# Kernel optimization log

Hardware: AMD Instinct MI355X
Metric: run time of the kernel (lower is better)

## Reference

```python
import jax, jax.numpy as jnp
import numpy as np

T, B, A, N = 64, 32, 8, 16
E, H = 64, 4
LSTM_I, LSTM_H = 128, 128
D_SELF = 16 + 9 * (32 - 2) + 4  # 290


def setup_inputs() -> dict:
    key = jax.random.key(0)
    ks = jax.random.split(key, 24)
    f32 = jnp.float32
    d = {}
    d["x_agent"] = jax.random.normal(ks[0], (T, B, A, 16), f32)
    d["x_lidar"] = jax.random.normal(ks[1], (T, B, A, 32), f32)
    d["x_safe_zone"] = jax.random.normal(ks[2], (T, B, A, 4), f32)
    d["x_ent0"] = jax.random.normal(ks[3], (T, B, A, N, 12), f32)
    d["x_ent1"] = jax.random.normal(ks[4], (T, B, A, N, 8), f32)
    d["mask0"] = jax.random.randint(ks[5], (T, B, A, N), 0, 2).astype(jnp.int32)
    d["mask1"] = jax.random.randint(ks[6], (T, B, A, N), 0, 2).astype(jnp.int32)
    d["done"] = jax.random.randint(ks[7], (T, B), 0, 2).astype(jnp.int32)
    d["actions"] = jax.random.randint(ks[8], (T, B, A, 2), 0, 5).astype(jnp.int32)
    w = lambda k, s: jax.random.normal(k, s, f32) * 0.05
    z = lambda s: jnp.zeros(s, f32)
    d["conv_w"] = w(ks[9], (9, 1, 3)); d["conv_b"] = z((9,))
    d["self_w"] = w(ks[10], (E, 2 * D_SELF)); d["self_b"] = z((E,))
    d["ent0_w"] = w(ks[11], (E, 12 + D_SELF)); d["ent0_b"] = z((E,))
    d["ent1_w"] = w(ks[12], (E, 8 + D_SELF)); d["ent1_b"] = z((E,))
    d["in_proj_w"] = w(ks[13], (3 * E, E)); d["in_proj_b"] = z((3 * E,))
    d["out_proj_w"] = w(ks[14], (E, E)); d["out_proj_b"] = z((E,))
    d["sa_w"] = w(ks[15], (E, E)); d["sa_b"] = z((E,))
    d["pool_w"] = w(ks[16], (LSTM_I, D_SELF + E)); d["pool_b"] = z((LSTM_I,))
    d["w_ih"] = w(ks[17], (4 * LSTM_H, LSTM_I)); d["w_hh"] = w(ks[18], (4 * LSTM_H, LSTM_H))
    d["b_ih"] = z((4 * LSTM_H,)); d["b_hh"] = z((4 * LSTM_H,))
    d["head0_w"] = w(ks[19], (5, LSTM_H)); d["head0_b"] = z((5,))
    d["head1_w"] = w(ks[20], (5, LSTM_H)); d["head1_b"] = z((5,))
    return d


def _forward(x_agent, x_lidar, x_safe_zone, x_ent0, x_ent1,
             conv_w, conv_b, self_w, self_b, ent0_w, ent0_b, ent1_w, ent1_b,
             in_proj_w, in_proj_b, out_proj_w, out_proj_b, sa_w, sa_b,
             pool_w, pool_b, w_ih, w_hh, b_ih, b_hh,
             head0_w, head0_b, head1_w, head1_b,
             mask0, mask1, done, actions):
    f32 = jnp.float32
    lin = lambda x, w, b: x @ w.T + b
    # lidar conv: Conv1d(1,9,k=3), padding=0 (padding_mode='circular' is inert with padding=0)
    xl = x_lidar.reshape(T * B * A, 1, 32)
    zl = jax.lax.conv_general_dilated(xl, conv_w, (1,), 'VALID',
                                      dimension_numbers=('NCH', 'OIH', 'NCH'))
    zl = jax.nn.relu(zl + conv_b[None, :, None]).reshape(T, B, A, -1)  # (T,B,A,270)
    x_self = jnp.concatenate([x_agent, zl, x_safe_zone], axis=-1)  # (T,B,A,290)
    z_self = jax.nn.relu(lin(jnp.concatenate([x_self, x_self], -1), self_w, self_b))[..., None, :]
    xs = jnp.broadcast_to(x_self[..., None, :], (T, B, A, N, D_SELF))
    z0 = jax.nn.relu(lin(jnp.concatenate([x_ent0, xs], -1), ent0_w, ent0_b))
    z1 = jax.nn.relu(lin(jnp.concatenate([x_ent1, xs], -1), ent1_w, ent1_b))
    z_ent = jnp.concatenate([z_self, z0, z1], axis=-2)  # (T,B,A,M,E), M = 1+2N = 33
    M = z_ent.shape[-2]
    mask = jnp.concatenate([jnp.ones((T, B, A, 1), f32),
                            mask0.astype(f32), mask1.astype(f32)], axis=-1)  # (T,B,A,M)
    # self-attention over entities, flattened over (T,B,A)
    S = T * B * A
    zf = z_ent.reshape(S, M, E)
    q, k, v = jnp.split(zf @ in_proj_w.T + in_proj_b, 3, axis=-1)
    Dh = E // H
    q = q.reshape(S, M, H, Dh); k = k.reshape(S, M, H, Dh); v = v.reshape(S, M, H, Dh)
    sc = jnp.einsum('sqhd,skhd->shqk', q, k) / np.float32(np.sqrt(Dh))
    valid = mask.reshape(S, M) > 0
    sc = jnp.where(valid[:, None, None, :], sc, jnp.float32(-1e9))
    attn = jax.nn.softmax(sc, axis=-1)
    o = jnp.einsum('shqk,skhd->sqhd', attn, v).reshape(S, M, E)
    o = (o @ out_proj_w.T + out_proj_b).reshape(T, B, A, M, E)
    res = z_ent + jax.nn.relu(lin(o, sa_w, sa_b))
    z_pool = jnp.mean(res * mask[..., None], axis=-2)  # torch.mean over entity dim (divide by M)
    zin = jax.nn.relu(lin(jnp.concatenate([x_self, z_pool], -1), pool_w, pool_b))  # (T,B,A,128)
    # LSTM scan with done-based state resets (PyTorch gate order i,f,g,o)
    zin_f = zin.reshape(T, B * A, LSTM_I)
    done_f = jnp.repeat(done.astype(f32), A, axis=-1)  # (T, B*A)
    def step(carry, inp):
        h, c = carry
        x_t, d_t = inp
        keep = (1.0 - d_t)[:, None]
        h = h * keep
        c = c * keep
        g = x_t @ w_ih.T + b_ih + h @ w_hh.T + b_hh
        i, f, gg, og = jnp.split(g, 4, axis=-1)
        c = jax.nn.sigmoid(f) * c + jax.nn.sigmoid(i) * jnp.tanh(gg)
        h = jax.nn.sigmoid(og) * jnp.tanh(c)
        return (h, c), h
    h0 = jnp.zeros((B * A, LSTM_H), f32)
    c0 = jnp.zeros((B * A, LSTM_H), f32)
    _, hs = jax.lax.scan(step, (h0, c0), (zin_f, done_f))
    z_lstm = hs.reshape(T, B, A, LSTM_H)
    # categorical heads: per-head logprob of given action and entropy
    lps, ents = [], []
    for i, (hw, hb) in enumerate(((head0_w, head0_b), (head1_w, head1_b))):
        logp = jax.nn.log_softmax(lin(z_lstm, hw, hb), axis=-1)
        p = jnp.exp(logp)
        ents.append(-(p * logp).sum(-1))
        lps.append(jnp.take_along_axis(logp, actions[..., i:i + 1], axis=-1)[..., 0])
    logprobs = lps[0] * lps[1]  # .prod(dim=-1) over heads as in source
    entropies = jnp.stack(ents, axis=-1)
    return logprobs, entropies


def reference(x_agent, x_lidar, x_safe_zone, x_ent0, x_ent1, mask0, mask1, done, actions,
              conv_w, conv_b, self_w, self_b, ent0_w, ent0_b, ent1_w, ent1_b,
              in_proj_w, in_proj_b, out_proj_w, out_proj_b, sa_w, sa_b,
              pool_w, pool_b, w_ih, w_hh, b_ih, b_hh,
              head0_w, head0_b, head1_w, head1_b):
    logprobs, entropies = _forward(x_agent, x_lidar, x_safe_zone, x_ent0, x_ent1,
                                   conv_w, conv_b, self_w, self_b, ent0_w, ent0_b,
                                   ent1_w, ent1_b, in_proj_w, in_proj_b, out_proj_w,
                                   out_proj_b, sa_w, sa_b, pool_w, pool_b,
                                   w_ih, w_hh, b_ih, b_hh,
                                   head0_w, head0_b, head1_w, head1_b,
                                   mask0, mask1, done, actions)
    return (actions, logprobs, entropies)
```

## Files before the change

kernel.cpp:

```cpp
#include <hip/hip_runtime.h>
#include <hip/hip_bf16.h>
#include <math.h>

#define T_DIM 64
#define B_DIM 32
#define S_TOT 16384
#define BA 256
#define FN_SB 16

#define ACT_OFF 0
#define LP_OFF 32768
#define ENT_OFF 49152

typedef __attribute__((ext_vector_type(8))) short short8;
typedef __attribute__((ext_vector_type(4))) float f32x4;
typedef unsigned int uint32;

__device__ __forceinline__ float sigf(float x) { return 1.0f / (1.0f + expf(-x)); }
__device__ __forceinline__ float bf2f(unsigned short u) {
    union { unsigned int i; float f; } a; a.i = ((unsigned int)u) << 16; return a.f;
}
__device__ __forceinline__ uint32 pkbf(float a, float b) {
    __hip_bfloat16 ha = __float2bfloat16(a), hb = __float2bfloat16(b);
    return (uint32)(*(unsigned short*)&ha) | ((uint32)(*(unsigned short*)&hb) << 16);
}
__device__ __forceinline__ short f2bs(float v) {
    __hip_bfloat16 h = __float2bfloat16(v); return *(short*)&h;
}
__device__ __forceinline__ int pswz(int row) { return (((row & 3) ^ ((row >> 2) & 3)) << 4); }

__global__ __launch_bounds__(256) void k_cvt2(
    const float* __restrict__ inp_w, const float* __restrict__ outp_w,
    const float* __restrict__ outp_b, const float* __restrict__ sa_w,
    const float* __restrict__ sa_b, const float* __restrict__ self_w,
    const float* __restrict__ pool_w, const float* __restrict__ ent0_w,
    const float* __restrict__ ent1_w, const float* __restrict__ w_ih,
    const float* __restrict__ w_hh,
    short* __restrict__ wq, short* __restrict__ Wf,
    short* __restrict__ We0, short* __restrict__ We1,
    short* __restrict__ wos, float* __restrict__ bos,
    short* __restrict__ wihb, short* __restrict__ whhb,
    short* __restrict__ wp2)
{
    int i = blockIdx.x * 256 + threadIdx.x;
    if (i < 12288) wq[i] = f2bs(inp_w[i]);
    if (i < 65536) { wihb[i] = f2bs(w_ih[i]); whhb[i] = f2bs(w_hh[i]); }
    if (i < 8192) { int c = i >> 6, k = i & 63; wp2[i] = f2bs(pool_w[(size_t)c * 354 + 290 + k]); }
    if (i < 4096) {
        int c = i >> 6, k = i & 63;
        float s = 0.f;
        for (int j = 0; j < 64; ++j) s = fmaf(sa_w[c * 64 + j], outp_w[j * 64 + k], s);
        wos[i] = f2bs(s);
    }
    if (i < 64) {
        float s = sa_b[i];
        for (int j = 0; j < 64; ++j) s = fmaf(sa_w[i * 64 + j], outp_b[j], s);
        bos[i] = s;
    }
    if (i < 1024) {
        int cp = i >> 4, k = i & 15;
        int ct = cp >> 4, lr2 = cp & 15;
        int e = 32 * (ct >> 1) + 2 * lr2 + (ct & 1);
        We0[i] = f2bs(k < 12 ? ent0_w[e * 302 + k] : 0.f);
        We1[i] = f2bs(k < 8 ? ent1_w[e * 298 + k] : 0.f);
    }
    if (i < 102400) {
        int c = i / 320, k = i - c * 320;
        float v = 0.f;
        if (k < 290) {
            if (c < 64) v = self_w[c * 580 + k] + self_w[c * 580 + 290 + k];
            else if (c < 192) v = pool_w[(size_t)(c - 64) * 354 + k];
            else if (c < 256) v = ent0_w[(c - 192) * 302 + 12 + k];
            else v = ent1_w[(c - 256) * 298 + 8 + k];
        }
        Wf[i] = f2bs(v);
    }
}

#define FN_XSB 0
#define FN_XP0 16384
#define FN_XP1 20736
#define FN_TOTAL 25088

__global__ __launch_bounds__(256, 4) void k_frontN(
    const float* __restrict__ xag, const float* __restrict__ xlid,
    const float* __restrict__ xsz, const float* __restrict__ xe0,
    const float* __restrict__ xe1,
    const float* __restrict__ conv_w, const float* __restrict__ conv_b,
    const float* __restrict__ self_b, const float* __restrict__ ent0_b,
    const float* __restrict__ ent1_b,
    const short* __restrict__ Wf, const short* __restrict__ We0,
    const short* __restrict__ We1,
    __hip_bfloat16* __restrict__ z_ent, float* __restrict__ zin_x)
{
    extern __shared__ char smem[];
    char* xsb = smem + FN_XSB;
    float* xp0f = (float*)(smem + FN_XP0);
    float* xp1f = (float*)(smem + FN_XP1);
    char* ae = smem + FN_XSB;
    float* lidf = (float*)(smem + FN_XP0);

    const int tid = threadIdx.x;
    const int s0 = blockIdx.x * FN_SB;
    const int wv = __builtin_amdgcn_readfirstlane(tid >> 6);
    const int l = tid & 63;
    const int lr = l & 15;
    const int lg = l >> 4;

    for (int i = tid; i < FN_SB * 32; i += 256) {
        int d = i & 31, sl = i >> 5;
        lidf[d * 18 + sl] = xlid[(size_t)s0 * 32 + i];
    }
    for (int i = tid; i < FN_SB * 16; i += 256) {
        int sl = i >> 4, d = i & 15;
        *(short*)(xsb + ((sl * 640 + d * 2) ^ ((sl & 7) << 4))) = f2bs(xag[(size_t)s0 * 16 + i]);
    }
    for (int i = tid; i < FN_SB * 4; i += 256) {
        int sl = i >> 2, d = i & 3;
        *(short*)(xsb + ((sl * 640 + (286 + d) * 2) ^ ((sl & 7) << 4))) = f2bs(xsz[(size_t)s0 * 4 + i]);
    }
    for (int i = tid; i < FN_SB * 30; i += 256) {
        int sl = i / 30, d = 290 + (i - (i / 30) * 30);
        *(short*)(xsb + ((sl * 640 + d * 2) ^ ((sl & 7) << 4))) = 0;
    }
    __syncthreads();
    #pragma unroll
    for (int c = 0; c < 9; ++c) {
        float w0 = conv_w[c * 3], w1 = conv_w[c * 3 + 1], w2 = conv_w[c * 3 + 2];
        float bb = conv_b[c];
        for (int i = tid; i < 30 * FN_SB; i += 256) {
            int p = i >> 4, sl = i & 15;
            float v = bb + w0 * lidf[p * 18 + sl] + w1 * lidf[(p + 1) * 18 + sl]
                    + w2 * lidf[(p + 2) * 18 + sl];
            *(short*)(xsb + ((sl * 640 + (16 + c * 30 + p) * 2) ^ ((sl & 7) << 4))) = f2bs(fmaxf(v, 0.f));
        }
    }
    __syncthreads();

    f32x4 acc[5];
    #pragma unroll
    for (int c = 0; c < 5; ++c) acc[c] = (f32x4){0.f, 0.f, 0.f, 0.f};

    for (int kk = 0; kk < 10; ++kk) {
        short8 af = *(const short8*)(xsb + ((lr * 640 + kk * 64 + lg * 16) ^ ((lr & 7) << 4)));
        short8 bf[5];
        #pragma unroll
        for (int c = 0; c < 5; ++c) {
            int col = (wv * 5 + c) * 16 + lr;
            bf[c] = *(const short8*)(Wf + (size_t)col * 320 + kk * 32 + lg * 8);
        }
        #pragma unroll
        for (int c = 0; c < 5; ++c)
            acc[c] = __builtin_amdgcn_mfma_f32_16x16x32_bf16(af, bf[c], acc[c], 0, 0, 0);
    }

    #pragma unroll
    for (int c = 0; c < 5; ++c) {
        int ct = wv * 5 + c;
        int gc = ct * 16 + lr;
        int rowb = lg * 4;
        f32x4 a = acc[c];
        if (ct * 16 < 64) {
            float bias = self_b[gc];
            #pragma unroll
            for (int r = 0; r < 4; ++r)
                z_ent[(size_t)(s0 + rowb + r) * 2112 + gc] = __float2bfloat16(fmaxf(a[r] + bias, 0.f));
        } else if (ct * 16 < 192) {
            int r2 = gc - 64;
            #pragma unroll
            for (int r = 0; r < 4; ++r)
                zin_x[(size_t)(s0 + rowb + r) * 128 + r2] = a[r];
        } else if (ct * 16 < 256) {
            float bias = ent0_b[gc - 192];
            #pragma unroll
            for (int r = 0; r < 4; ++r)
                xp0f[(rowb + r) * 68 + (gc - 192)] = a[r] + bias;
        } else {
            float bias = ent1_b[gc - 256];
            #pragma unroll
            for (int r = 0; r < 4; ++r)
                xp1f[(rowb + r) * 68 + (gc - 256)] = a[r] + bias;
        }
    }
    __syncthreads();

    {
        short8 bz = {0, 0, 0, 0, 0, 0, 0, 0};
        short8 be[4];
        #pragma unroll
        for (int ct = 0; ct < 4; ++ct) {
            int col = ct * 16 + lr;
            short8 bv = *(const short8*)(We0 + col * 16 + (lg & 1) * 8);
            be[ct] = (lg < 2) ? bv : bz;
        }
        for (int i = tid; i < 4096; i += 256) ((uint32*)ae)[i] = 0;
        __syncthreads();
        {
            int sl = tid >> 4, n = tid & 15;
            int row = sl * 16 + n;
            int sw = (row & 3) << 4;
            const float4* src = (const float4*)(xe0 + (size_t)(s0 + sl) * 192 + n * 12);
            float4 v0 = src[0], v1 = src[1], v2 = src[2];
            *(uint32*)(ae + ((row * 64 + 0) ^ sw))  = pkbf(v0.x, v0.y);
            *(uint32*)(ae + ((row * 64 + 4) ^ sw))  = pkbf(v0.z, v0.w);
            *(uint32*)(ae + ((row * 64 + 8) ^ sw))  = pkbf(v1.x, v1.y);
            *(uint32*)(ae + ((row * 64 + 12) ^ sw)) = pkbf(v1.z, v1.w);
            *(uint32*)(ae + ((row * 64 + 16) ^ sw)) = pkbf(v2.x, v2.y);
            *(uint32*)(ae + ((row * 64 + 20) ^ sw)) = pkbf(v2.z, v2.w);
        }
        __syncthreads();
        #pragma unroll
        for (int j = 0; j < 4; ++j) {
            int gs = wv * 4 + j;
            int row = gs * 16 + lr;
            short8 af = *(const short8*)(ae + ((row * 64 + lg * 16) ^ ((row & 3) << 4)));
            f32x4 a2[4];
            #pragma unroll
            for (int ct = 0; ct < 4; ++ct) {
                f32x4 z = {0.f, 0.f, 0.f, 0.f};
                a2[ct] = __builtin_amdgcn_mfma_f32_16x16x32_bf16(af, be[ct], z, 0, 0, 0);
            }
            #pragma unroll
            for (int t = 0; t < 2; ++t) {
                int e0 = 32 * t + 2 * lr;
                float xv0 = xp0f[gs * 68 + e0];
                float xv1 = xp0f[gs * 68 + e0 + 1];
                #pragma unroll
                for (int r = 0; r < 4; ++r) {
                    int n = lg * 4 + r;
                    float v0 = fmaxf(a2[2 * t][r] + xv0, 0.f);
                    float v1 = fmaxf(a2[2 * t + 1][r] + xv1, 0.f);
                    *(uint32*)((char*)z_ent + ((size_t)(s0 + gs) * 2112 + (1 + n) * 64 + e0) * 2) = pkbf(v0, v1);
                }
            }
        }
        __syncthreads();
    }

    {
        short8 bz = {0, 0, 0, 0, 0, 0, 0, 0};
        short8 be[4];
        #pragma unroll
        for (int ct = 0; ct < 4; ++ct) {
            int col = ct * 16 + lr;
            short8 bv = *(const short8*)(We1 + col * 16 + (lg & 1) * 8);
            be[ct] = (lg < 2) ? bv : bz;
        }
        for (int i = tid; i < 4096; i += 256) ((uint32*)ae)[i] = 0;
        __syncthreads();
        {
            int sl = tid >> 4, n = tid & 15;
            int row = sl * 16 + n;
            int sw = (row & 3) << 4;
            const float4* src = (const float4*)(xe1 + (size_t)(s0 + sl) * 128 + n * 8);
            float4 v0 = src[0], v1 = src[1];
            *(uint32*)(ae + ((row * 64 + 0) ^ sw))  = pkbf(v0.x, v0.y);
            *(uint32*)(ae + ((row * 64 + 4) ^ sw))  = pkbf(v0.z, v0.w);
            *(uint32*)(ae + ((row * 64 + 8) ^ sw))  = pkbf(v1.x, v1.y);
            *(uint32*)(ae + ((row * 64 + 12) ^ sw)) = pkbf(v1.z, v1.w);
        }
        __syncthreads();
        #pragma unroll
        for (int j = 0; j < 4; ++j) {
            int gs = wv * 4 + j;
            int row = gs * 16 + lr;
            short8 af = *(const short8*)(ae + ((row * 64 + lg * 16) ^ ((row & 3) << 4)));
            f32x4 a2[4];
            #pragma unroll
            for (int ct = 0; ct < 4; ++ct) {
                f32x4 z = {0.f, 0.f, 0.f, 0.f};
                a2[ct] = __builtin_amdgcn_mfma_f32_16x16x32_bf16(af, be[ct], z, 0, 0, 0);
            }
            #pragma unroll
            for (int t = 0; t < 2; ++t) {
                int e0 = 32 * t + 2 * lr;
                float xv0 = xp1f[gs * 68 + e0];
                float xv1 = xp1f[gs * 68 + e0 + 1];
                #pragma unroll
                for (int r = 0; r < 4; ++r) {
                    int n = lg * 4 + r;
                    float v0 = fmaxf(a2[2 * t][r] + xv0, 0.f);
                    float v1 = fmaxf(a2[2 * t + 1][r] + xv1, 0.f);
                    *(uint32*)((char*)z_ent + ((size_t)(s0 + gs) * 2112 + (17 + n) * 64 + e0) * 2) = pkbf(v0, v1);
                }
            }
        }
    }
}

#define AG_QB   0
#define AG_KB   4224
#define AG_VT   8448
#define AG_PW   12544
#define AG_P32  16640
#define AG_V32  17408
#define AG_MSK  17664
#define AG_TOTAL 17824

__global__ __launch_bounds__(256, 8) void k_attnG(
    const __hip_bfloat16* __restrict__ z_ent,
    const int* __restrict__ mask0, const int* __restrict__ mask1,
    const short* __restrict__ wqkvb, const float* __restrict__ inp_b,
    const short* __restrict__ wos_g, const float* __restrict__ bos_g,
    float* __restrict__ pooled_ws)
{
    extern __shared__ char smem[];
    char*  Qb  = smem + AG_QB;
    char*  Kb  = smem + AG_KB;
    char*  Vt  = smem + AG_VT;
    char*  Pw  = smem + AG_PW;
    float* P32 = (float*)(smem + AG_P32);
    float* V32 = (float*)(smem + AG_V32);
    float* msk = (float*)(smem + AG_MSK);
    char*  ob  = Qb;

    const int tid = threadIdx.x;
    const int s = blockIdx.x;
    const short* zg = (const short*)(z_ent + (size_t)s * 2112);

    if (tid < 16) msk[1 + tid] = (float)mask0[(size_t)s * 16 + tid];
    else if (tid < 32) msk[17 + (tid - 16)] = (float)mask1[(size_t)s * 16 + (tid - 16)];
    else if (tid == 32) msk[0] = 1.0f;

    const int wv = __builtin_amdgcn_readfirstlane(tid >> 6);
    const int l  = tid & 63;
    const int lr = l & 15;
    const int lg = l >> 4;

    {
        short8 bw[3][2]; float bias[3];
        #pragma unroll
        for (int c = 0; c < 3; ++c) {
            int col = (wv * 3 + c) * 16 + lr;
            bw[c][0] = *(const short8*)(wqkvb + col * 64 + lg * 8);
            bw[c][1] = *(const short8*)(wqkvb + col * 64 + 32 + lg * 8);
            bias[c] = inp_b[col];
        }
        for (int rt = 0; rt < 3; ++rt) {
            int arow = rt * 16 + lr;
            if (arow > 32) arow = 32;
            short8 a0 = *(const short8*)(zg + arow * 64 + lg * 8);
            short8 a1 = *(const short8*)(zg + arow * 64 + 32 + lg * 8);
            #pragma unroll
            for (int c = 0; c < 3; ++c) {
                f32x4 acc = {0.f, 0.f, 0.f, 0.f};
                acc = __builtin_amdgcn_mfma_f32_16x16x32_bf16(a0, bw[c][0], acc, 0, 0, 0);
                acc = __builtin_amdgcn_mfma_f32_16x16x32_bf16(a1, bw[c][1], acc, 0, 0, 0);
                int col = (wv * 3 + c) * 16 + lr;
                int rb = rt * 16 + lg * 4;
                #pragma unroll
                for (int r = 0; r < 4; ++r) {
                    int q = rb + r;
                    if (q < 33) {
                        float val = acc[r] + bias[c];
                        if (col < 64) {
                            int h = col >> 4, d = col & 15;
                            *(short*)(Qb + ((h * 33 + q) * 32) + d * 2) = f2bs(val);
                        } else if (col < 128) {
                            int kc = col - 64; int h = kc >> 4, d = kc & 15;
                            *(short*)(Kb + ((h * 33 + q) * 32) + d * 2) = f2bs(val);
                        } else {
                            int vc = col - 128; int h = vc >> 4, d = vc & 15;
                            if (q < 32)
                                *(short*)(Vt + (h * 16 + d) * 64 + ((q * 2) ^ pswz(d))) = f2bs(val);
                            else
                                V32[h * 16 + d] = val;
                        }
                    }
                }
            }
        }
    }
    __syncthreads();

    uint32 pk[3][4];
    {
        const short8 zero8 = {0, 0, 0, 0, 0, 0, 0, 0};
        short8 kf[3];
        #pragma unroll
        for (int t = 0; t < 3; ++t)
            kf[t] = (lg < 2) ? *(const short8*)(Kb + ((wv * 33 + t * 16 + lr) * 32) + lg * 16) : zero8;
        float mk0 = msk[lr];
        float mk1 = msk[16 + lr];
        float mk2 = (lr == 0) ? msk[32] : 0.f;
        float sc0 = mk0 * 0.25f, bo0 = (mk0 - 1.f) * 40.f;
        float sc1 = mk1 * 0.25f, bo1 = (mk1 - 1.f) * 40.f;
        float sc2 = mk2 * 0.25f, bo2 = (mk2 - 1.f) * 40.f;
        #pragma unroll
        for (int qt = 0; qt < 3; ++qt) {
            short8 qf = (lg < 2) ? *(const short8*)(Qb + ((wv * 33 + qt * 16 + lr) * 32) + lg * 16) : zero8;
            f32x4 z = {0.f, 0.f, 0.f, 0.f};
            f32x4 S0 = __builtin_amdgcn_mfma_f32_16x16x32_bf16(qf, kf[0], z, 0, 0, 0);
            f32x4 S1 = __builtin_amdgcn_mfma_f32_16x16x32_bf16(qf, kf[1], z, 0, 0, 0);
            f32x4 S2 = __builtin_amdgcn_mfma_f32_16x16x32_bf16(qf, kf[2], z, 0, 0, 0);
            #pragma unroll
            for (int r = 0; r < 4; ++r) {
                float e0 = __expf(fmaf(S0[r], sc0, bo0));
                float e1 = __expf(fmaf(S1[r], sc1, bo1));
                float e2 = __expf(fmaf(S2[r], sc2, bo2));
                float sm = e0 + e1 + e2;
                sm += __shfl_xor(sm, 1);
                sm += __shfl_xor(sm, 2);
                sm += __shfl_xor(sm, 4);
                sm += __shfl_xor(sm, 8);
                float inv = 1.0f / sm;
                pk[qt][r] = pkbf(e0 * inv, e1 * inv);
                if (lr == 0) P32[wv * 48 + qt * 16 + lg * 4 + r] = e2 * inv;
            }
        }
    }
    __syncthreads();

    {
        short8 vf = *(const short8*)(Vt + (wv * 16 + lr) * 64 + ((lg * 16) ^ pswz(lr)));
        float v32reg = V32[wv * 16 + lr];
        f32x4 C[3];
        #pragma unroll
        for (int qt = 0; qt < 3; ++qt) {
            #pragma unroll
            for (int r = 0; r < 4; ++r) {
                int ql = lg * 4 + r;
                uint32 p = pk[qt][r];
                char* prow = Pw + wv * 1024 + ql * 64;
                int sz = pswz(ql);
                *(short*)(prow + ((lr * 2) ^ sz)) = (short)(p & 0xffffu);
                *(short*)(prow + (((16 + lr) * 2) ^ sz)) = (short)(p >> 16);
            }
            short8 pf = *(const short8*)(Pw + wv * 1024 + lr * 64 + ((lg * 16) ^ pswz(lr)));
            f32x4 z = {0.f, 0.f, 0.f, 0.f};
            C[qt] = __builtin_amdgcn_mfma_f32_16x16x32_bf16(pf, vf, z, 0, 0, 0);
        }
        #pragma unroll
        for (int qt = 0; qt < 3; ++qt) {
            #pragma unroll
            for (int r = 0; r < 4; ++r) {
                int q = qt * 16 + lg * 4 + r;
                if (q <= 32) {
                    float cv = C[qt][r] + P32[wv * 48 + q] * v32reg;
                    *(short*)(ob + ((q * 128 + (wv * 16 + lr) * 2) ^ ((q & 7) << 4))) = f2bs(cv);
                }
            }
        }
    }
    __syncthreads();

    {
        int col = wv * 16 + lr;
        short8 b0 = *(const short8*)(wos_g + col * 64 + lg * 8);
        short8 b1 = *(const short8*)(wos_g + col * 64 + 32 + lg * 8);
        float bias = bos_g[col];
        float ps = 0.f;
        for (int rt = 0; rt < 3; ++rt) {
            int arow = rt * 16 + lr;
            int sw = (arow & 7) << 4;
            short8 a0 = *(const short8*)(ob + ((arow * 128 + lg * 16) ^ sw));
            short8 a1 = *(const short8*)(ob + ((arow * 128 + 64 + lg * 16) ^ sw));
            f32x4 acc = {0.f, 0.f, 0.f, 0.f};
            acc = __builtin_amdgcn_mfma_f32_16x16x32_bf16(a0, b0, acc, 0, 0, 0);
            acc = __builtin_amdgcn_mfma_f32_16x16x32_bf16(a1, b1, acc, 0, 0, 0);
            int rb = rt * 16 + lg * 4;
            #pragma unroll
            for (int r = 0; r < 4; ++r) {
                int row = rb + r;
                if (row < 33) {
                    float zev = bf2f(*(const unsigned short*)(zg + row * 64 + col));
                    ps += msk[row] * (zev + fmaxf(acc[r] + bias, 0.f));
                }
            }
        }
        ps += __shfl_xor(ps, 16); ps += __shfl_xor(ps, 32);
        if (lg == 0) pooled_ws[(size_t)s * 64 + col] = ps * (1.0f / 33.0f);
    }
}

__global__ __launch_bounds__(256, 2) void k_zinx(
    const float* __restrict__ pooled_ws, const float* __restrict__ zin_x,
    const short* __restrict__ wp2, const float* __restrict__ pool_b,
    const short* __restrict__ wihb, const float* __restrict__ b_ih,
    const float* __restrict__ b_hh, short* __restrict__ xp)
{
    extern __shared__ char smem[];
    char* A1 = smem;
    char* zt = smem + 8192;
    const int tid = threadIdx.x;
    const size_t r0 = (size_t)blockIdx.x * 64;

    for (int i = tid; i < 2048; i += 256) {
        int sl = i >> 5, dp = i & 31;
        float2 v = ((const float2*)(pooled_ws + (r0 + sl) * 64))[dp];
        *(uint32*)(A1 + ((sl * 128 + dp * 4) ^ ((sl & 7) << 4))) = pkbf(v.x, v.y);
    }
    __syncthreads();

    const int wv = __builtin_amdgcn_readfirstlane(tid >> 6);
    const int l = tid & 63;
    const int lr = l & 15;
    const int lg = l >> 4;

    #pragma unroll
    for (int c = 0; c < 2; ++c) {
        int col = (wv * 2 + c) * 16 + lr;
        short8 bf0 = *(const short8*)(wp2 + col * 64 + lg * 8);
        short8 bf1 = *(const short8*)(wp2 + col * 64 + 32 + lg * 8);
        float bias = pool_b[col];
        #pragma unroll
        for (int rt = 0; rt < 4; ++rt) {
            int row16 = rt * 16 + lr;
            short8 a0 = *(const short8*)(A1 + ((row16 * 128 + lg * 16) ^ ((row16 & 7) << 4)));
            short8 a1 = *(const short8*)(A1 + ((row16 * 128 + 64 + lg * 16) ^ ((row16 & 7) << 4)));
            f32x4 acc = {0.f, 0.f, 0.f, 0.f};
            acc = __builtin_amdgcn_mfma_f32_16x16x32_bf16(a0, bf0, acc, 0, 0, 0);
            acc = __builtin_amdgcn_mfma_f32_16x16x32_bf16(a1, bf1, acc, 0, 0, 0);
            #pragma unroll
            for (int r = 0; r < 4; ++r) {
                int row = rt * 16 + lg * 4 + r;
                float v = fmaxf(acc[r] + bias + zin_x[(r0 + row) * 128 + col], 0.f);
                *(short*)(zt + ((row * 256 + col * 2) ^ ((row & 7) << 4))) = f2bs(v);
            }
        }
    }
    __syncthreads();

    short8 af[4][4];
    #pragma unroll
    for (int rt = 0; rt < 4; ++rt)
        #pragma unroll
        for (int kc = 0; kc < 4; ++kc) {
            int row = rt * 16 + lr;
            af[rt][kc] = *(const short8*)(zt + ((row * 256 + kc * 64 + lg * 16) ^ ((row & 7) << 4)));
        }

    for (int ct8 = 0; ct8 < 8; ++ct8) {
        int ct = wv * 8 + ct8;
        int col = ct * 16 + lr;
        short8 bf[4];
        #pragma unroll
        for (int kc = 0; kc < 4; ++kc)
            bf[kc] = *(const short8*)(wihb + (size_t)col * 128 + kc * 32 + lg * 8);
        float bias = b_ih[col] + b_hh[col];
        int g = col >> 7, j = col & 127;
        #pragma unroll
        for (int rt = 0; rt < 4; ++rt) {
            f32x4 acc = {0.f, 0.f, 0.f, 0.f};
            #pragma unroll
            for (int kc = 0; kc < 4; ++kc)
                acc = __builtin_amdgcn_mfma_f32_16x16x32_bf16(af[rt][kc], bf[kc], acc, 0, 0, 0);
            #pragma unroll
            for (int r = 0; r < 4; ++r)
                xp[(r0 + rt * 16 + lg * 4 + r) * 512 + j * 4 + g] = f2bs(acc[r] + bias);
        }
    }
}

__global__ __launch_bounds__(512, 1) void k_lstm2(
    const short* __restrict__ xp, const short* __restrict__ whhb,
    const int* __restrict__ done, float* __restrict__ h_all)
{
    __shared__ short hl[16 * 128];
    __shared__ float keepl[64 * 16];
    const int tid = threadIdx.x;
    const int s0 = blockIdx.x * 16;
    const int wv = __builtin_amdgcn_readfirstlane(tid >> 6);
    const int l = tid & 63;
    const int lr = l & 15;
    const int lg = l >> 4;

    for (int i = tid; i < 1024; i += 512) {
        int t = i >> 4, ls = i & 15;
        keepl[i] = done[t * 32 + ((s0 + ls) >> 3)] ? 0.f : 1.f;
    }
    for (int i = tid; i < 1024; i += 512) ((uint32*)hl)[i] = 0;

    short8 bf[4][4];
    #pragma unroll
    for (int gi = 0; gi < 4; ++gi) {
        int col = (gi * 8 + wv) * 16 + lr;
        #pragma unroll
        for (int kc = 0; kc < 4; ++kc)
            bf[gi][kc] = *(const short8*)(whhb + (size_t)col * 128 + kc * 32 + lg * 8);
    }
    float c0 = 0.f, c1 = 0.f, c2 = 0.f, c3 = 0.f;
    const int jcol = wv * 16 + lr;

    short4 xn[4];
    #pragma unroll
    for (int r = 0; r < 4; ++r)
        xn[r] = *(const short4*)(xp + ((size_t)(s0 + lg * 4 + r)) * 512 + jcol * 4);
    __syncthreads();

    for (int t = 0; t < T_DIM; ++t) {
        short4 xc[4];
        #pragma unroll
        for (int r = 0; r < 4; ++r) xc[r] = xn[r];
        if (t < 63) {
            #pragma unroll
            for (int r = 0; r < 4; ++r)
                xn[r] = *(const short4*)(xp + ((size_t)(t + 1) * 256 + s0 + lg * 4 + r) * 512 + jcol * 4);
        }
        short8 af[4];
        #pragma unroll
        for (int kc = 0; kc < 4; ++kc)
            af[kc] = *(const short8*)((char*)hl + ((lr * 256 + kc * 64 + lg * 16) ^ ((lr & 7) << 4)));
        f32x4 z = {0.f, 0.f, 0.f, 0.f};
        f32x4 Ci = z, Cf = z, Cg = z, Co = z;
        #pragma unroll
        for (int kc = 0; kc < 4; ++kc) {
            Ci = __builtin_amdgcn_mfma_f32_16x16x32_bf16(af[kc], bf[0][kc], Ci, 0, 0, 0);
            Cf = __builtin_amdgcn_mfma_f32_16x16x32_bf16(af[kc], bf[1][kc], Cf, 0, 0, 0);
            Cg = __builtin_amdgcn_mfma_f32_16x16x32_bf16(af[kc], bf[2][kc], Cg, 0, 0, 0);
            Co = __builtin_amdgcn_mfma_f32_16x16x32_bf16(af[kc], bf[3][kc], Co, 0, 0, 0);
        }
        __syncthreads();

        #pragma unroll
        for (int r = 0; r < 4; ++r) {
            int sl = lg * 4 + r;
            float kt = keepl[t * 16 + sl];
            float gi = bf2f((unsigned short)xc[r].x) + Ci[r];
            float gf = bf2f((unsigned short)xc[r].y) + Cf[r];
            float gg = bf2f((unsigned short)xc[r].z) + Cg[r];
            float go = bf2f((unsigned short)xc[r].w) + Co[r];
            float cc = (r == 0 ? c0 : r == 1 ? c1 : r == 2 ? c2 : c3) * kt;
            cc = sigf(gf) * cc + sigf(gi) * tanhf(gg);
            float hn = sigf(go) * tanhf(cc);
            if (r == 0) c0 = cc; else if (r == 1) c1 = cc; else if (r == 2) c2 = cc; else c3 = cc;
            float kn = (t < 63) ? keepl[(t + 1) * 16 + sl] : 1.f;
            *(short*)((char*)hl + ((sl * 256 + jcol * 2) ^ ((sl & 7) << 4))) = f2bs(hn * kn);
            h_all[((size_t)t * 256 + s0 + sl) * 128 + jcol] = hn;
        }
        __syncthreads();
    }
}

__global__ __launch_bounds__(256) void k_heads(
    const float* __restrict__ h_all, const int* __restrict__ actions,
    const float* __restrict__ h0w, const float* __restrict__ h0b,
    const float* __restrict__ h1w, const float* __restrict__ h1b,
    float* __restrict__ out)
{
    __shared__ float w0[640], w1[640], b0[8], b1[8];
    const int tid = threadIdx.x;
    for (int i = tid; i < 640; i += 256) { w0[i] = h0w[i]; w1[i] = h1w[i]; }
    if (tid < 5) { b0[tid] = h0b[tid]; b1[tid] = h1b[tid]; }
    __syncthreads();
    const int g = blockIdx.x * 256 + tid;
    const float* h = h_all + (size_t)g * 128;
    float l0[5], l1[5];
    #pragma unroll
    for (int cc = 0; cc < 5; ++cc) { l0[cc] = b0[cc]; l1[cc] = b1[cc]; }
    for (int j = 0; j < 128; ++j) {
        float hv = h[j];
        #pragma unroll
        for (int cc = 0; cc < 5; ++cc) {
            l0[cc] = fmaf(w0[cc * 128 + j], hv, l0[cc]);
            l1[cc] = fmaf(w1[cc * 128 + j], hv, l1[cc]);
        }
    }
    int a0 = actions[(size_t)g * 2], a1 = actions[(size_t)g * 2 + 1];
    float m0 = l0[0], m1 = l1[0];
    #pragma unroll
    for (int cc = 1; cc < 5; ++cc) { m0 = fmaxf(m0, l0[cc]); m1 = fmaxf(m1, l1[cc]); }
    float s0 = 0.f, s1 = 0.f;
    #pragma unroll
    for (int cc = 0; cc < 5; ++cc) { s0 += expf(l0[cc] - m0); s1 += expf(l1[cc] - m1); }
    float lse0 = m0 + logf(s0), lse1 = m1 + logf(s1);
    float ent0 = 0.f, ent1 = 0.f, lp0 = 0.f, lp1 = 0.f;
    #pragma unroll
    for (int cc = 0; cc < 5; ++cc) {
        float p0 = l0[cc] - lse0, p1 = l1[cc] - lse1;
        ent0 -= expf(p0) * p0;
        ent1 -= expf(p1) * p1;
        if (cc == a0) lp0 = p0;
        if (cc == a1) lp1 = p1;
    }
    out[ACT_OFF + (size_t)g * 2]     = (float)a0;
    out[ACT_OFF + (size_t)g * 2 + 1] = (float)a1;
    out[LP_OFF + g]                  = lp0 * lp1;
    out[ENT_OFF + (size_t)g * 2]     = ent0;
    out[ENT_OFF + (size_t)g * 2 + 1] = ent1;
}

extern "C" void kernel_launch(void* const* d_in, const int* in_sizes, int n_in,
                              void* d_out, int out_size, void* d_ws, size_t ws_size,
                              hipStream_t stream)
{
    const float* x_agent = (const float*)d_in[0];
    const float* x_lidar = (const float*)d_in[1];
    const float* x_safe  = (const float*)d_in[2];
    const float* x_ent0  = (const float*)d_in[3];
    const float* x_ent1  = (const float*)d_in[4];
    const int*   mask0   = (const int*)d_in[5];
    const int*   mask1   = (const int*)d_in[6];
    const int*   done    = (const int*)d_in[7];
    const int*   actions = (const int*)d_in[8];
    const float* conv_w  = (const float*)d_in[9];
    const float* conv_b  = (const float*)d_in[10];
    const float* self_w  = (const float*)d_in[11];
    const float* self_b  = (const float*)d_in[12];
    const float* ent0_w  = (const float*)d_in[13];
    const float* ent0_b  = (const float*)d_in[14];
    const float* ent1_w  = (const float*)d_in[15];
    const float* ent1_b  = (const float*)d_in[16];
    const float* inp_w   = (const float*)d_in[17];
    const float* inp_b   = (const float*)d_in[18];
    const float* outp_w  = (const float*)d_in[19];
    const float* outp_b  = (const float*)d_in[20];
    const float* sa_w    = (const float*)d_in[21];
    const float* sa_b    = (const float*)d_in[22];
    const float* pool_w  = (const float*)d_in[23];
    const float* pool_b  = (const float*)d_in[24];
    const float* w_ih    = (const float*)d_in[25];
    const float* w_hh    = (const float*)d_in[26];
    const float* b_ih    = (const float*)d_in[27];
    const float* b_hh    = (const float*)d_in[28];
    const float* h0w     = (const float*)d_in[29];
    const float* h0b     = (const float*)d_in[30];
    const float* h1w     = (const float*)d_in[31];
    const float* h1b     = (const float*)d_in[32];

    __hip_bfloat16* z_ent = (__hip_bfloat16*)d_ws;
    float* zin_x  = (float*)((char*)d_ws + (size_t)S_TOT * 2112 * 2);
    float* pooled = zin_x + (size_t)S_TOT * 128;
    float* h_all  = pooled + (size_t)S_TOT * 64;
    short* xp     = (short*)(h_all + (size_t)S_TOT * 128);
    short* wqkvb  = xp + (size_t)S_TOT * 512;
    short* Wf     = wqkvb + 12288;
    short* We0    = Wf + 102400;
    short* We1    = We0 + 1024;
    short* wos    = We1 + 1024;
    float* bos    = (float*)(wos + 4096);
    short* wihb   = (short*)(bos + 64);
    short* whhb   = wihb + 65536;
    short* wp2    = whhb + 65536;

    k_cvt2<<<400, 256, 0, stream>>>(inp_w, outp_w, outp_b, sa_w, sa_b, self_w, pool_w,
                                    ent0_w, ent1_w, w_ih, w_hh,
                                    wqkvb, Wf, We0, We1, wos, bos, wihb, whhb, wp2);

    k_frontN<<<S_TOT / FN_SB, 256, FN_TOTAL, stream>>>(
        x_agent, x_lidar, x_safe, x_ent0, x_ent1,
        conv_w, conv_b, self_b, ent0_b, ent1_b,
        Wf, We0, We1, z_ent, zin_x);

    k_attnG<<<S_TOT, 256, AG_TOTAL, stream>>>(
        z_ent, mask0, mask1, wqkvb, inp_b, wos, bos, pooled);

    k_zinx<<<256, 256, 24576, stream>>>(pooled, zin_x, wp2, pool_b, wihb, b_ih, b_hh, xp);

    k_lstm2<<<16, 512, 0, stream>>>(xp, whhb, done, h_all);

    k_heads<<<S_TOT / 256, 256, 0, stream>>>(h_all, actions, h0w, h0b, h1w, h1b, (float*)d_out);
}
```

Before: 318.1 us.

## Double-buffer LSTM hidden state and vectorize QKV/attention output stores

In the LSTM recurrence, the hidden-state shared buffer is double-buffered, which removes one of the two barriers per timestep. In the attention kernel, the QKV projection is restructured so each wave computes one Q, K and V tile. Q and K use swapped MFMA operands (transposed output) so results can be written as vectorized short4 stores instead of scattered 2-byte stores. The PV product is likewise transposed to allow short4 output stores, at the cost of more intricate indexing that must stay consistent with the layouts downstream.

```diff
diff --git a/kernel.cpp b/kernel.cpp
--- a/kernel.cpp
+++ b/kernel.cpp
@@ -328,46 +328,48 @@
     const int lg = l >> 4;
 
     {
-        short8 bw[3][2]; float bias[3];
-        #pragma unroll
-        for (int c = 0; c < 3; ++c) {
-            int col = (wv * 3 + c) * 16 + lr;
-            bw[c][0] = *(const short8*)(wqkvb + col * 64 + lg * 8);
-            bw[c][1] = *(const short8*)(wqkvb + col * 64 + 32 + lg * 8);
-            bias[c] = inp_b[col];
-        }
+        int colQ = wv * 16 + lr;
+        short8 wQ0 = *(const short8*)(wqkvb + colQ * 64 + lg * 8);
+        short8 wQ1 = *(const short8*)(wqkvb + colQ * 64 + 32 + lg * 8);
+        int colK = (wv + 4) * 16 + lr;
+        short8 wK0 = *(const short8*)(wqkvb + colK * 64 + lg * 8);
+        short8 wK1 = *(const short8*)(wqkvb + colK * 64 + 32 + lg * 8);
+        int colV = (wv + 8) * 16 + lr;
+        short8 wV0 = *(const short8*)(wqkvb + colV * 64 + lg * 8);
+        short8 wV1 = *(const short8*)(wqkvb + colV * 64 + 32 + lg * 8);
+        float4 bQ = *(const float4*)(inp_b + wv * 16 + lg * 4);
+        float4 bK = *(const float4*)(inp_b + 64 + wv * 16 + lg * 4);
+        float biasV = inp_b[128 + wv * 16 + lr];
         for (int rt = 0; rt < 3; ++rt) {
             int arow = rt * 16 + lr;
             if (arow > 32) arow = 32;
             short8 a0 = *(const short8*)(zg + arow * 64 + lg * 8);
             short8 a1 = *(const short8*)(zg + arow * 64 + 32 + lg * 8);
-            #pragma unroll
-            for (int c = 0; c < 3; ++c) {
-                f32x4 acc = {0.f, 0.f, 0.f, 0.f};
-                acc = __builtin_amdgcn_mfma_f32_16x16x32_bf16(a0, bw[c][0], acc, 0, 0, 0);
-                acc = __builtin_amdgcn_mfma_f32_16x16x32_bf16(a1, bw[c][1], acc, 0, 0, 0);
-                int col = (wv * 3 + c) * 16 + lr;
-                int rb = rt * 16 + lg * 4;
-                #pragma unroll
-                for (int r = 0; r < 4; ++r) {
-                    int q = rb + r;
-                    if (q < 33) {
-                        float val = acc[r] + bias[c];
-                        if (col < 64) {
-                            int h = col >> 4, d = col & 15;
-                            *(short*)(Qb + ((h * 33 + q) * 32) + d * 2) = f2bs(val);
-                        } else if (col < 128) {
-                            int kc = col - 64; int h = kc >> 4, d = kc & 15;
-                            *(short*)(Kb + ((h * 33 + q) * 32) + d * 2) = f2bs(val);
-                        } else {
-                            int vc = col - 128; int h = vc >> 4, d = vc & 15;
-                            if (q < 32)
-                                *(short*)(Vt + (h * 16 + d) * 64 + ((q * 2) ^ pswz(d))) = f2bs(val);
-                            else
-                                V32[h * 16 + d] = val;
-                        }
-                    }
-                }
+            f32x4 z4 = {0.f, 0.f, 0.f, 0.f};
+            f32x4 aQ = __builtin_amdgcn_mfma_f32_16x16x32_bf16(wQ0, a0, z4, 0, 0, 0);
+            aQ = __builtin_amdgcn_mfma_f32_16x16x32_bf16(wQ1, a1, aQ, 0, 0, 0);
+            f32x4 aK = __builtin_amdgcn_mfma_f32_16x16x32_bf16(wK0, a0, z4, 0, 0, 0);
+            aK = __builtin_amdgcn_mfma_f32_16x16x32_bf16(wK1, a1, aK, 0, 0, 0);
+            f32x4 aV = __builtin_amdgcn_mfma_f32_16x16x32_bf16(a0, wV0, z4, 0, 0, 0);
+            aV = __builtin_amdgcn_mfma_f32_16x16x32_bf16(a1, wV1, aV, 0, 0, 0);
+            int q = rt * 16 + lr;
+            if (q < 33) {
+                short4 st;
+                st.x = f2bs(aQ[0] + bQ.x); st.y = f2bs(aQ[1] + bQ.y);
+                st.z = f2bs(aQ[2] + bQ.z); st.w = f2bs(aQ[3] + bQ.w);
+                *(short4*)(Qb + (wv * 33 + q) * 32 + lg * 8) = st;
+                st.x = f2bs(aK[0] + bK.x); st.y = f2bs(aK[1] + bK.y);
+                st.z = f2bs(aK[2] + bK.z); st.w = f2bs(aK[3] + bK.w);
+                *(short4*)(Kb + (wv * 33 + q) * 32 + lg * 8) = st;
+            }
+            if (rt < 2) {
+                int q0 = rt * 16 + lg * 4;
+                short4 sv;
+                sv.x = f2bs(aV[0] + biasV); sv.y = f2bs(aV[1] + biasV);
+                sv.z = f2bs(aV[2] + biasV); sv.w = f2bs(aV[3] + biasV);
+                *(short4*)(Vt + (wv * 16 + lr) * 64 + ((q0 * 2) ^ pswz(lr))) = sv;
+            } else if (lg == 0) {
+                V32[wv * 16 + lr] = aV[0] + biasV;
             }
         }
     }
@@ -413,7 +415,7 @@
 
     {
         short8 vf = *(const short8*)(Vt + (wv * 16 + lr) * 64 + ((lg * 16) ^ pswz(lr)));
-        float v32reg = V32[wv * 16 + lr];
+        float4 v32v = *(const float4*)(V32 + wv * 16 + lg * 4);
         f32x4 C[3];
         #pragma unroll
         for (int qt = 0; qt < 3; ++qt) {
@@ -428,17 +430,19 @@
             }
             short8 pf = *(const short8*)(Pw + wv * 1024 + lr * 64 + ((lg * 16) ^ pswz(lr)));
             f32x4 z = {0.f, 0.f, 0.f, 0.f};
-            C[qt] = __builtin_amdgcn_mfma_f32_16x16x32_bf16(pf, vf, z, 0, 0, 0);
+            C[qt] = __builtin_amdgcn_mfma_f32_16x16x32_bf16(vf, pf, z, 0, 0, 0);
         }
         #pragma unroll
         for (int qt = 0; qt < 3; ++qt) {
-            #pragma unroll
-            for (int r = 0; r < 4; ++r) {
-                int q = qt * 16 + lg * 4 + r;
-                if (q <= 32) {
-                    float cv = C[qt][r] + P32[wv * 48 + q] * v32reg;
-                    *(short*)(ob + ((q * 128 + (wv * 16 + lr) * 2) ^ ((q & 7) << 4))) = f2bs(cv);
-                }
+            int q = qt * 16 + lr;
+            if (q <= 32) {
+                float p32 = P32[wv * 48 + q];
+                short4 o;
+                o.x = f2bs(C[qt][0] + p32 * v32v.x);
+                o.y = f2bs(C[qt][1] + p32 * v32v.y);
+                o.z = f2bs(C[qt][2] + p32 * v32v.z);
+                o.w = f2bs(C[qt][3] + p32 * v32v.w);
+                *(short4*)(ob + ((q * 128 + (wv * 16 + lg * 4) * 2) ^ ((q & 7) << 4))) = o;
             }
         }
     }
@@ -556,7 +560,7 @@
     const short* __restrict__ xp, const short* __restrict__ whhb,
     const int* __restrict__ done, float* __restrict__ h_all)
 {
-    __shared__ short hl[16 * 128];
+    __shared__ short hl[2][16 * 128];
     __shared__ float keepl[64 * 16];
     const int tid = threadIdx.x;
     const int s0 = blockIdx.x * 16;
@@ -569,7 +573,7 @@
         int t = i >> 4, ls = i & 15;
         keepl[i] = done[t * 32 + ((s0 + ls) >> 3)] ? 0.f : 1.f;
     }
-    for (int i = tid; i < 1024; i += 512) ((uint32*)hl)[i] = 0;
+    for (int i = tid; i < 1024; i += 512) ((uint32*)hl[0])[i] = 0;
 
     short8 bf[4][4];
     #pragma unroll
@@ -589,6 +593,8 @@
     __syncthreads();
 
     for (int t = 0; t < T_DIM; ++t) {
+        char* hr = (char*)hl[t & 1];
+        char* hw = (char*)hl[(t + 1) & 1];
         short4 xc[4];
         #pragma unroll
         for (int r = 0; r < 4; ++r) xc[r] = xn[r];
@@ -600,7 +606,7 @@
         short8 af[4];
         #pragma unroll
         for (int kc = 0; kc < 4; ++kc)
-            af[kc] = *(const short8*)((char*)hl + ((lr * 256 + kc * 64 + lg * 16) ^ ((lr & 7) << 4)));
+            af[kc] = *(const short8*)(hr + ((lr * 256 + kc * 64 + lg * 16) ^ ((lr & 7) << 4)));
         f32x4 z = {0.f, 0.f, 0.f, 0.f};
         f32x4 Ci = z, Cf = z, Cg = z, Co = z;
         #pragma unroll
@@ -610,7 +616,6 @@
             Cg = __builtin_amdgcn_mfma_f32_16x16x32_bf16(af[kc], bf[2][kc], Cg, 0, 0, 0);
             Co = __builtin_amdgcn_mfma_f32_16x16x32_bf16(af[kc], bf[3][kc], Co, 0, 0, 0);
         }
-        __syncthreads();
 
         #pragma unroll
         for (int r = 0; r < 4; ++r) {
@@ -625,7 +630,7 @@
             float hn = sigf(go) * tanhf(cc);
             if (r == 0) c0 = cc; else if (r == 1) c1 = cc; else if (r == 2) c2 = cc; else c3 = cc;
             float kn = (t < 63) ? keepl[(t + 1) * 16 + sl] : 1.f;
-            *(short*)((char*)hl + ((sl * 256 + jcol * 2) ^ ((sl & 7) << 4))) = f2bs(hn * kn);
+            *(short*)(hw + ((sl * 256 + jcol * 2) ^ ((sl & 7) << 4))) = f2bs(hn * kn);
             h_all[((size_t)t * 256 + s0 + sl) * 128 + jcol] = hn;
         }
         __syncthreads();
```

After: 325.7 us. 1.02x slower.
